# Optimization experiments

Hardware: AMD Instinct MI355X
Metric: run time of the kernel (lower is better)

The kernel has to match this reference:

```python
import jax, jax.numpy as jnp
import numpy as np
import math

N = 30000        # nodes
E = 390000       # edges (first N are self-loops, in node order)
H = 64
NNS = 4          # num_node_states
NES = 4          # num_edge_states
NGRAPH = 64      # graphs in batch
TEMP_ON_EVAL = 1.0


def from_binary(bits):
    # bits: [..., k] of {0,1} -> integer code sum(bits * 2^k)
    pw = (2 ** jnp.arange(bits.shape[-1])).astype(bits.dtype)
    return jnp.sum(bits * pw, axis=-1)


def segment_softmax(logits, seg, num_seg, tau):
    m = jax.ops.segment_max(logits, seg, num_segments=num_seg)
    e = jnp.exp((logits - m[seg]) / tau)
    s = jax.ops.segment_sum(e, seg, num_segments=num_seg)
    return e / s[seg]


def segment_hard_onehot(logits, seg, num_seg):
    # gumbel_softmax with tau=0, no noise: one-hot at per-segment argmax (first on ties)
    n = logits.shape[0]
    m = jax.ops.segment_max(logits, seg, num_segments=num_seg)
    idx = jnp.where(logits >= m[seg], jnp.arange(n, dtype=jnp.int32), jnp.int32(n))
    first = jax.ops.segment_min(idx, seg, num_segments=num_seg)
    return (jnp.arange(n, dtype=jnp.int32) == first[seg]).astype(jnp.int32)


def select_best(emb, bits, scalars, index, num_index):
    # SelectBest with use_select_best=True. states are even ints < 2^(k+1);
    # unique((states, index)) groups == fused key states*num_index+index.
    states = 2 * from_binary(bits)
    key = states * num_index + index
    num_key = (2 ** (bits.shape[-1] + 1)) * num_index
    best = segment_hard_onehot(-scalars[:, 0], key, num_key)
    return emb[states + best]


def temp_by_step(step, upper, lower, num_iter, temp_on_eval):
    if step == -1:
        return temp_on_eval
    frac = min(float(step) / num_iter, 1.0)
    return upper + (lower - upper) * frac


def forward(node_states, edge_states, scalars, edge_index, batch_vec, rev_idx,
            emb_edge, emb_sbv, emb_sbr, emb_static,
            Wq, Wk, Wv, Wek, Wev, Wc, training_step):
    ei0, ei1 = edge_index[0], edge_index[1]
    # self-loop edges are the first N edges in node order ->
    # scalars[edge_index[0]==edge_index[1]] == scalars[:N]
    node_scalars = scalars[:N]                                   # [N,1]

    # select_best_from_virtual
    node_fts = select_best(emb_sbv, node_states, node_scalars, batch_vec, NGRAPH)  # [N,H]
    edge_fts = emb_edge[from_binary(edge_states)]                # [E,H]

    Q = node_fts @ Wq.T
    K = node_fts @ Wk.T
    V = node_fts @ Wv.T

    # combined_edge_KV
    sb = select_best(emb_sbr, node_states[ei0], scalars, ei1, N)  # [E,H]
    edge_K = sb @ Wek.T
    sender_s = node_scalars[ei0]                                  # [E,1]
    reciever_s = node_scalars[ei1]                                # [E,1]
    rlx = (scalars < reciever_s)
    rlx_d = (sender_s + scalars < reciever_s)
    fts = jnp.concatenate([rlx, rlx_d], axis=-1).astype(jnp.int32)  # [E,2] bits
    static_fts = emb_static[from_binary(fts)]                     # [E,H]
    combined = jnp.concatenate([edge_fts, edge_fts[rev_idx], static_fts], axis=1)  # [E,3H]
    edge_V = combined @ Wc.T                                      # [E,H]

    # compute_message
    Qe = Q[ei1]
    Ke = K[ei0] + edge_K
    Ve = V[ei0] + edge_V
    alpha = jnp.sum(Qe * Ke, axis=-1) / math.sqrt(H)              # [E]
    tau = temp_by_step(int(training_step), 3.0, 0.1, 10000, TEMP_ON_EVAL)
    alpha = segment_softmax(alpha, ei1, N, tau)
    message = Ve * alpha[:, None]                                  # [E,H]

    node_out = node_fts + jax.ops.segment_sum(message, ei1, num_segments=N)
    edge_out = edge_fts + message
    return node_out, edge_out


def setup_inputs() -> dict:
    key = jax.random.key(0)
    ks = jax.random.split(key, 16)
    node_states = jax.random.randint(ks[0], (N, NNS), 0, 2, dtype=jnp.int32)
    edge_states = jax.random.randint(ks[1], (E, NES), 0, 2, dtype=jnp.int32)
    scalars = jax.random.normal(ks[2], (E, 1), dtype=jnp.float32)
    loops = jnp.arange(N, dtype=jnp.int32)
    senders = jax.random.randint(ks[3], (E - N,), 0, N, dtype=jnp.int32)
    receivers = jax.random.randint(ks[4], (E - N,), 0, N, dtype=jnp.int32)
    edge_index = jnp.stack([jnp.concatenate([loops, senders]),
                            jnp.concatenate([loops, receivers])])  # [2,E]
    batch_vec = jnp.sort(jax.random.randint(ks[5], (N,), 0, NGRAPH, dtype=jnp.int32))
    rev_idx = jax.random.permutation(ks[6], E).astype(jnp.int32)
    s = 0.05
    return {
        'node_states': node_states, 'edge_states': edge_states, 'scalars': scalars,
        'edge_index': edge_index, 'batch_vec': batch_vec, 'rev_idx': rev_idx,
        'emb_edge': s * jax.random.normal(ks[7], (2 ** NES, H), dtype=jnp.float32),
        'emb_sbv': s * jax.random.normal(ks[8], (2 ** (NNS + 1), H), dtype=jnp.float32),
        'emb_sbr': s * jax.random.normal(ks[9], (2 ** (NNS + 1), H), dtype=jnp.float32),
        'emb_static': s * jax.random.normal(ks[10], (4, H), dtype=jnp.float32),
        'Wq': s * jax.random.normal(ks[11], (H, H), dtype=jnp.float32),
        'Wk': s * jax.random.normal(ks[12], (H, H), dtype=jnp.float32),
        'Wv': s * jax.random.normal(ks[13], (H, H), dtype=jnp.float32),
        'Wek': s * jax.random.normal(ks[14], (H, H), dtype=jnp.float32),
        'Wev': s * jax.random.normal(ks[15], (H, H), dtype=jnp.float32),
        'Wc': s * jax.random.normal(jax.random.fold_in(key, 99), (H, 3 * H), dtype=jnp.float32),
        'training_step': -1,
    }


def reference(node_states, edge_states, scalars, edge_index, batch_vec, rev_idx,
              emb_edge, emb_sbv, emb_sbr, emb_static,
              Wq, Wk, Wv, Wek, Wev, Wc, training_step):
    return forward(node_states, edge_states, scalars, edge_index, batch_vec, rev_idx,
                   emb_edge, emb_sbv, emb_sbr, emb_static,
                   Wq, Wk, Wv, Wek, Wev, Wc, training_step)
```

## Files before the change

### kernel.cpp

```cpp
#include <hip/hip_runtime.h>

#define NN 30000
#define NE 390000
#define HH 64
#define NGRAPH 64
#define AGG_BLOCKS 1024
#define NB 118

__device__ __forceinline__ unsigned sortable_f32(float f) {
    unsigned u = __float_as_uint(f);
    return (u & 0x80000000u) ? ~u : (u | 0x80000000u);
}

#define T_V   0
#define T_C1  2048
#define T_C2  3072
#define T_C3  4096
#define T_A   4352
#define T_B   5376
#define T_Q   6400
#define T_K   8448
#define T_EK  10496

__global__ void k_tab1(const float* __restrict__ emb_sbv, const float* __restrict__ emb_sbr,
                       const float* __restrict__ emb_edge, const float* __restrict__ emb_static,
                       const float* __restrict__ Wq, const float* __restrict__ Wk,
                       const float* __restrict__ Wv, const float* __restrict__ Wek,
                       const float* __restrict__ Wc, float* __restrict__ tabs) {
    int idx = blockIdx.x * 256 + threadIdx.x;
    if (idx >= 10496) return;
    float acc = 0.f;
    if (idx < 2048) {
        int r = idx >> 6, h = idx & 63;
        for (int j = 0; j < 64; ++j) acc += emb_sbv[r*64+j] * Wv[h*64+j];
        tabs[T_V + idx] = acc;
    } else if (idx < 3072) {
        int t = idx - 2048; int r = t >> 6, h = t & 63;
        for (int j = 0; j < 64; ++j) acc += emb_edge[r*64+j] * Wc[h*192+j];
        tabs[T_C1 + t] = acc;
    } else if (idx < 4096) {
        int t = idx - 3072; int r = t >> 6, h = t & 63;
        for (int j = 0; j < 64; ++j) acc += emb_edge[r*64+j] * Wc[h*192+64+j];
        tabs[T_C2 + t] = acc;
    } else if (idx < 4352) {
        int t = idx - 4096; int r = t >> 6, h = t & 63;
        for (int j = 0; j < 64; ++j) acc += emb_static[r*64+j] * Wc[h*192+128+j];
        tabs[T_C3 + t] = acc;
    } else if (idx < 6400) {
        int t = idx - 4352; int r = t >> 6, h = t & 63;
        for (int j = 0; j < 64; ++j) acc += emb_sbv[r*64+j] * Wq[h*64+j];
        tabs[T_Q + t] = acc;
    } else if (idx < 8448) {
        int t = idx - 6400; int r = t >> 6, h = t & 63;
        for (int j = 0; j < 64; ++j) acc += emb_sbv[r*64+j] * Wk[h*64+j];
        tabs[T_K + t] = acc;
    } else {
        int t = idx - 8448; int r = t >> 6, h = t & 63;
        for (int j = 0; j < 64; ++j) acc += emb_sbr[r*64+j] * Wek[h*64+j];
        tabs[T_EK + t] = acc;
    }
}

__global__ void k_tab2(float* __restrict__ tabs) {
    int idx = blockIdx.x * 256 + threadIdx.x;
    if (idx >= 2048) return;
    const float* TQ = tabs + T_Q;
    float acc = 0.f;
    if (idx < 1024) {
        int r1 = idx >> 5, r0 = idx & 31;
        const float* TK = tabs + T_K;
        for (int j = 0; j < 64; ++j) acc += TQ[r1*64+j] * TK[r0*64+j];
        tabs[T_A + idx] = acc * 0.125f;
    } else {
        int t = idx - 1024; int r1 = t >> 5, rk = t & 31;
        const float* TEK = tabs + T_EK;
        for (int j = 0; j < 64; ++j) acc += TQ[r1*64+j] * TEK[rk*64+j];
        tabs[T_B + t] = acc * 0.125f;
    }
}

__global__ void k_node1(const int4* __restrict__ node_states, const float* __restrict__ scalars,
                        const int* __restrict__ batch_vec, int* __restrict__ ns,
                        unsigned long long* __restrict__ nodeSel) {
    int i = blockIdx.x * 256 + threadIdx.x;
    if (i >= NN) return;
    int4 b = node_states[i];
    int st = 2 * (b.x + 2*b.y + 4*b.z + 8*b.w);
    ns[i] = st;
    int key = (st >> 1) * NGRAPH + batch_vec[i];
    unsigned long long pk = ((unsigned long long)sortable_f32(scalars[i]) << 32) | (unsigned)i;
    atomicMin(&nodeSel[key], pk);
}

__global__ void k_edge1(const int4* __restrict__ edge_states, const float* __restrict__ scalars,
                        const int* __restrict__ ei0, const int* __restrict__ ei1,
                        unsigned char* __restrict__ esi,
                        unsigned* __restrict__ cnt, unsigned* __restrict__ rank) {
    int e = blockIdx.x * 256 + threadIdx.x;
    if (e >= NE) return;
    int4 b = edge_states[e];
    int es = b.x + 2*b.y + 4*b.z + 8*b.w;
    float sc = scalars[e];
    int s0 = ei0[e], s1 = ei1[e];
    float send = scalars[s0], recv = scalars[s1];
    int si = (sc < recv ? 1 : 0) + (send + sc < recv ? 2 : 0);
    esi[e] = (unsigned char)(es | (si << 4));
    rank[e] = atomicAdd(&cnt[s1], 1u);
}

__global__ __launch_bounds__(256) void k_bsum(const unsigned* __restrict__ cnt,
                                              unsigned* __restrict__ bsum) {
    __shared__ unsigned red[256];
    int t = threadIdx.x;
    int i = blockIdx.x * 256 + t;
    red[t] = (i < NN) ? cnt[i] : 0u;
    __syncthreads();
    for (int o = 128; o > 0; o >>= 1) {
        if (t < o) red[t] += red[t + o];
        __syncthreads();
    }
    if (t == 0) bsum[blockIdx.x] = red[0];
}

__global__ __launch_bounds__(128) void k_sscan(const unsigned* __restrict__ bsum,
                                               unsigned* __restrict__ bbase,
                                               unsigned* __restrict__ base) {
    __shared__ unsigned s[128];
    int t = threadIdx.x;
    unsigned v = (t < NB) ? bsum[t] : 0u;
    s[t] = v;
    __syncthreads();
    for (int o = 1; o < 128; o <<= 1) {
        unsigned u = (t >= o) ? s[t - o] : 0u;
        __syncthreads();
        s[t] += u;
        __syncthreads();
    }
    if (t < NB) bbase[t] = s[t] - v;
    if (t == 127) { bbase[NB] = s[127]; base[NN] = s[127]; }
}

__global__ __launch_bounds__(256) void k_base(const unsigned* __restrict__ cnt,
        const unsigned* __restrict__ bbase, unsigned* __restrict__ base,
        const int* __restrict__ ns, const int* __restrict__ batch_vec,
        const unsigned long long* __restrict__ nodeSel, int* __restrict__ rowArr) {
    __shared__ unsigned s[256];
    int t = threadIdx.x;
    int i = blockIdx.x * 256 + t;
    unsigned v = (i < NN) ? cnt[i] : 0u;
    s[t] = v;
    __syncthreads();
    for (int o = 1; o < 256; o <<= 1) {
        unsigned u = (t >= o) ? s[t - o] : 0u;
        __syncthreads();
        s[t] += u;
        __syncthreads();
    }
    if (i < NN) {
        base[i] = bbase[blockIdx.x] + s[t] - v;
        int st = ns[i];
        int key = (st >> 1) * NGRAPH + batch_vec[i];
        unsigned win = (unsigned)(nodeSel[key] & 0xffffffffull);
        rowArr[i] = st + (win == (unsigned)i ? 1 : 0);
    }
}

__global__ __launch_bounds__(256) void k_edge2(const int* __restrict__ ei0,
        const int* __restrict__ ei1, const int* __restrict__ rowArr,
        const unsigned char* __restrict__ esi, const int* __restrict__ rev_idx,
        const float* __restrict__ scalars, const unsigned* __restrict__ base,
        const unsigned* __restrict__ rank, uint2* __restrict__ sKey,
        float* __restrict__ sScal) {
    int e = blockIdx.x * 256 + threadIdx.x;
    if (e >= NE) return;
    int s0 = ei0[e], s1 = ei1[e];
    unsigned r0w = (unsigned)rowArr[s0];
    unsigned stq = (r0w & ~1u) >> 1;
    unsigned inf = esi[e];
    unsigned infr = esi[rev_idx[e]];
    unsigned pos = base[s1] + rank[e];
    sKey[pos] = make_uint2((unsigned)e | (r0w << 19) | ((inf & 15u) << 24) | ((infr & 15u) << 28),
                           stq | ((inf >> 4) << 4));
    sScal[pos] = scalars[e];
}

__global__ __launch_bounds__(256) void k_agg(
        const unsigned* __restrict__ base, const uint2* __restrict__ sKey,
        const float* __restrict__ sScal, const int* __restrict__ rowArr,
        const float* __restrict__ tabs, const float* __restrict__ emb_edge,
        const float* __restrict__ emb_sbv, const int* __restrict__ step_ptr,
        float* __restrict__ out_node, float* __restrict__ out_edge) {
    __shared__ float lds[9472];
    __shared__ unsigned scr[4][32];
    int tid = threadIdx.x;
    for (int j = tid; j < 6400; j += 256) lds[j] = tabs[j];
    for (int j = tid; j < 1024; j += 256) lds[6400 + j] = emb_edge[j];
    for (int j = tid; j < 2048; j += 256) lds[7424 + j] = emb_sbv[j];
    __syncthreads();
    int step = step_ptr[0];
    float invTau;
    if (step == -1) invTau = 1.0f;
    else { float frac = fminf((float)step / 10000.f, 1.f); invTau = 1.0f / (3.0f + (0.1f - 3.0f) * frac); }
    int wid = tid >> 6, lane = tid & 63;
    unsigned* mySc = scr[wid];
    unsigned* myE  = scr[wid] + 16;
    int q = lane >> 4, cidx = (lane & 15) << 2;
    for (int i = blockIdx.x * 4 + wid; i < NN; i += AGG_BLOCKS * 4) {
        unsigned j0 = base[i], j1 = base[i + 1];
        int d = (int)(j1 - j0);
        int r1 = rowArr[i];
        const float* Arow = lds + T_A + r1 * 32;
        const float* Brow = lds + T_B + r1 * 32;
        float4 acc = {0.f, 0.f, 0.f, 0.f};
        if (lane < 16) { mySc[lane] = 0xffffffffu; myE[lane] = 0xffffffffu; }
        __builtin_amdgcn_sched_barrier(0);
        if (d > 0 && d <= 64) {
            bool act = lane < d;
            uint2 key = act ? sKey[j0 + lane] : make_uint2(0u, 0u);
            float sc  = act ? sScal[j0 + lane] : 0.f;
            unsigned scs = sortable_f32(sc);
            unsigned g = key.y & 15u;
            unsigned e19 = key.x & 0x7ffffu;
            if (act) atomicMin(&mySc[g], scs);
            __builtin_amdgcn_sched_barrier(0);
            unsigned ms = mySc[g];
            if (act && scs == ms) atomicMin(&myE[g], e19);
            __builtin_amdgcn_sched_barrier(0);
            bool win = act && (myE[g] == e19);
            int r0 = (key.x >> 19) & 31;
            int ekrow = ((int)(key.y & 15u) << 1) + (win ? 1 : 0);
            float ex = act ? __expf((Arow[r0] + Brow[ekrow]) * invTau) : 0.f;
            float s = ex;
            #pragma unroll
            for (int o = 1; o < 64; o <<= 1) s += __shfl_xor(s, o);
            float p = ex / s;
            int nIt = (d + 3) >> 2;
            for (int it = 0; it < nIt; ++it) {
                int jj = it * 4 + q;
                unsigned kx = __shfl(key.x, jj);
                unsigned ky = (unsigned)__shfl((int)key.y, jj);
                float pp = __shfl(p, jj);
                if (jj < d) {
                    unsigned e = kx & 0x7ffffu;
                    int rr0 = (kx >> 19) & 31, es = (kx >> 24) & 15, esr = (kx >> 28) & 15;
                    int si = (ky >> 4) & 3;
                    float4 tv = *(const float4*)&lds[(rr0 << 6) + cidx];
                    float4 c1 = *(const float4*)&lds[T_C1 + (es << 6) + cidx];
                    float4 c2 = *(const float4*)&lds[T_C2 + (esr << 6) + cidx];
                    float4 c3 = *(const float4*)&lds[T_C3 + (si << 6) + cidx];
                    float4 ee = *(const float4*)&lds[6400 + (es << 6) + cidx];
                    float4 o;
                    o.x = pp * (tv.x + c1.x + c2.x + c3.x);
                    o.y = pp * (tv.y + c1.y + c2.y + c3.y);
                    o.z = pp * (tv.z + c1.z + c2.z + c3.z);
                    o.w = pp * (tv.w + c1.w + c2.w + c3.w);
                    acc.x += o.x; acc.y += o.y; acc.z += o.z; acc.w += o.w;
                    o.x += ee.x; o.y += ee.y; o.z += ee.z; o.w += ee.w;
                    *(float4*)&out_edge[(size_t)e * 64 + cidx] = o;
                }
            }
        } else if (d > 64) {
            for (unsigned c = j0; c < j1; c += 64) {
                unsigned j = c + lane;
                if (j < j1) {
                    uint2 key = sKey[j];
                    atomicMin(&mySc[key.y & 15u], sortable_f32(sScal[j]));
                }
            }
            __builtin_amdgcn_sched_barrier(0);
            for (unsigned c = j0; c < j1; c += 64) {
                unsigned j = c + lane;
                if (j < j1) {
                    uint2 key = sKey[j];
                    unsigned g = key.y & 15u;
                    if (sortable_f32(sScal[j]) == mySc[g]) atomicMin(&myE[g], key.x & 0x7ffffu);
                }
            }
            __builtin_amdgcn_sched_barrier(0);
            float s = 0.f;
            for (unsigned c = j0; c < j1; c += 64) {
                unsigned j = c + lane;
                if (j < j1) {
                    uint2 key = sKey[j];
                    bool win = (myE[key.y & 15u] == (key.x & 0x7ffffu));
                    int r0 = (key.x >> 19) & 31;
                    int ekrow = ((int)(key.y & 15u) << 1) + (win ? 1 : 0);
                    s += __expf((Arow[r0] + Brow[ekrow]) * invTau);
                }
            }
            #pragma unroll
            for (int o = 1; o < 64; o <<= 1) s += __shfl_xor(s, o);
            float invS = 1.f / s;
            for (unsigned c = j0; c < j1; c += 4) {
                unsigned j = c + q;
                if (j < j1) {
                    uint2 key = sKey[j];
                    bool win = (myE[key.y & 15u] == (key.x & 0x7ffffu));
                    int r0 = (key.x >> 19) & 31;
                    int ekrow = ((int)(key.y & 15u) << 1) + (win ? 1 : 0);
                    float pp = __expf((Arow[r0] + Brow[ekrow]) * invTau) * invS;
                    unsigned e = key.x & 0x7ffffu;
                    int es = (key.x >> 24) & 15, esr = (key.x >> 28) & 15, si = (key.y >> 4) & 3;
                    float4 tv = *(const float4*)&lds[(r0 << 6) + cidx];
                    float4 c1 = *(const float4*)&lds[T_C1 + (es << 6) + cidx];
                    float4 c2 = *(const float4*)&lds[T_C2 + (esr << 6) + cidx];
                    float4 c3 = *(const float4*)&lds[T_C3 + (si << 6) + cidx];
                    float4 ee = *(const float4*)&lds[6400 + (es << 6) + cidx];
                    float4 o;
                    o.x = pp * (tv.x + c1.x + c2.x + c3.x);
                    o.y = pp * (tv.y + c1.y + c2.y + c3.y);
                    o.z = pp * (tv.z + c1.z + c2.z + c3.z);
                    o.w = pp * (tv.w + c1.w + c2.w + c3.w);
                    acc.x += o.x; acc.y += o.y; acc.z += o.z; acc.w += o.w;
                    o.x += ee.x; o.y += ee.y; o.z += ee.z; o.w += ee.w;
                    *(float4*)&out_edge[(size_t)e * 64 + cidx] = o;
                }
            }
        }
        acc.x += __shfl_xor(acc.x, 16); acc.y += __shfl_xor(acc.y, 16);
        acc.z += __shfl_xor(acc.z, 16); acc.w += __shfl_xor(acc.w, 16);
        acc.x += __shfl_xor(acc.x, 32); acc.y += __shfl_xor(acc.y, 32);
        acc.z += __shfl_xor(acc.z, 32); acc.w += __shfl_xor(acc.w, 32);
        if (lane < 16) {
            float4 nb = *(const float4*)&lds[7424 + (r1 << 6) + cidx];
            float4 o;
            o.x = nb.x + acc.x; o.y = nb.y + acc.y; o.z = nb.z + acc.z; o.w = nb.w + acc.w;
            *(float4*)&out_node[(size_t)i * 64 + cidx] = o;
        }
    }
}

extern "C" void kernel_launch(void* const* d_in, const int* in_sizes, int n_in,
                              void* d_out, int out_size, void* d_ws, size_t ws_size,
                              hipStream_t stream) {
    const int4*  node_states = (const int4*)d_in[0];
    const int4*  edge_states = (const int4*)d_in[1];
    const float* scalars     = (const float*)d_in[2];
    const int*   edge_index  = (const int*)d_in[3];
    const int*   batch_vec   = (const int*)d_in[4];
    const int*   rev_idx     = (const int*)d_in[5];
    const float* emb_edge    = (const float*)d_in[6];
    const float* emb_sbv     = (const float*)d_in[7];
    const float* emb_sbr     = (const float*)d_in[8];
    const float* emb_static  = (const float*)d_in[9];
    const float* Wq  = (const float*)d_in[10];
    const float* Wk  = (const float*)d_in[11];
    const float* Wv  = (const float*)d_in[12];
    const float* Wek = (const float*)d_in[13];
    const float* Wc  = (const float*)d_in[15];
    const int*   step = (const int*)d_in[16];

    const int* ei0 = edge_index;
    const int* ei1 = edge_index + NE;

    char* ws = (char*)d_ws;
    int*      ns     = (int*)(ws);
    int*      rowArr = (int*)(ws + 120000);
    unsigned char* esi = (unsigned char*)(ws + 240000);
    unsigned* rank   = (unsigned*)(ws + 630000);
    unsigned* cnt    = (unsigned*)(ws + 2190000);
    unsigned* baseA  = (unsigned*)(ws + 2310080);
    uint2*    sKey   = (uint2*)(ws + 2430144);
    float*    sScal  = (float*)(ws + 5550144);
    unsigned long long* nodeSel = (unsigned long long*)(ws + 7110144);
    float*    tabs   = (float*)(ws + 7118336);
    unsigned* bsum   = (unsigned*)(ws + 7168512);
    unsigned* bbase  = (unsigned*)(ws + 7169024);

    float* out_node = (float*)d_out;
    float* out_edge = out_node + (size_t)NN * HH;

    hipMemsetAsync(cnt, 0, NN * 4, stream);
    hipMemsetAsync(nodeSel, 0xFF, 1024 * 8, stream);

    hipLaunchKernelGGL(k_tab1, dim3(41), dim3(256), 0, stream,
                       emb_sbv, emb_sbr, emb_edge, emb_static, Wq, Wk, Wv, Wek, Wc, tabs);
    hipLaunchKernelGGL(k_tab2, dim3(8), dim3(256), 0, stream, tabs);

    int nb_node = NB;
    int nb_edge = (NE + 255) / 256;

    hipLaunchKernelGGL(k_node1, dim3(nb_node), dim3(256), 0, stream,
                       node_states, scalars, batch_vec, ns, nodeSel);
    hipLaunchKernelGGL(k_edge1, dim3(nb_edge), dim3(256), 0, stream,
                       edge_states, scalars, ei0, ei1, esi, cnt, rank);
    hipLaunchKernelGGL(k_bsum, dim3(NB), dim3(256), 0, stream, cnt, bsum);
    hipLaunchKernelGGL(k_sscan, dim3(1), dim3(128), 0, stream, bsum, bbase, baseA);
    hipLaunchKernelGGL(k_base, dim3(NB), dim3(256), 0, stream,
                       cnt, bbase, baseA, ns, batch_vec, nodeSel, rowArr);
    hipLaunchKernelGGL(k_edge2, dim3(nb_edge), dim3(256), 0, stream,
                       ei0, ei1, rowArr, esi, rev_idx, scalars, baseA, rank, sKey, sScal);
    hipLaunchKernelGGL(k_agg, dim3(AGG_BLOCKS), dim3(256), 0, stream,
                       baseA, sKey, sScal, rowArr, tabs, emb_edge, emb_sbv, step,
                       out_node, out_edge);
}
```

Measured before the change: 92.83 us.

## Merge preprocessing kernels into phased launches and move edge-side compute into aggregation

Collapses the table, node and edge preprocessing kernels plus the two memsets into three multi-role launches (init, phase2, phase3), cutting launch count and serial dependencies. Node row and scalar are packed into one uint2 per node. The sender scalar now rides in the sort key, so the aggregation kernel computes the static-index bits instead of the edge pass gathering sender and receiver scalars. The group id is derived from the row bits. The cost is extra ALU work inside the aggregation kernel and tighter coupling of key bit layouts.

```diff
diff --git a/kernel.cpp b/kernel.cpp
--- a/kernel.cpp
+++ b/kernel.cpp
@@ -5,7 +5,8 @@
 #define HH 64
 #define NGRAPH 64
 #define AGG_BLOCKS 1024
-#define NB 118
+#define NE_BLK 1524
+#define NN_BLK 118
 
 __device__ __forceinline__ unsigned sortable_f32(float f) {
     unsigned u = __float_as_uint(f);
@@ -22,104 +23,131 @@
 #define T_K   8448
 #define T_EK  10496
 
-__global__ void k_tab1(const float* __restrict__ emb_sbv, const float* __restrict__ emb_sbr,
-                       const float* __restrict__ emb_edge, const float* __restrict__ emb_static,
-                       const float* __restrict__ Wq, const float* __restrict__ Wk,
-                       const float* __restrict__ Wv, const float* __restrict__ Wek,
-                       const float* __restrict__ Wc, float* __restrict__ tabs) {
-    int idx = blockIdx.x * 256 + threadIdx.x;
-    if (idx >= 10496) return;
-    float acc = 0.f;
-    if (idx < 2048) {
-        int r = idx >> 6, h = idx & 63;
-        for (int j = 0; j < 64; ++j) acc += emb_sbv[r*64+j] * Wv[h*64+j];
-        tabs[T_V + idx] = acc;
-    } else if (idx < 3072) {
-        int t = idx - 2048; int r = t >> 6, h = t & 63;
-        for (int j = 0; j < 64; ++j) acc += emb_edge[r*64+j] * Wc[h*192+j];
-        tabs[T_C1 + t] = acc;
-    } else if (idx < 4096) {
-        int t = idx - 3072; int r = t >> 6, h = t & 63;
-        for (int j = 0; j < 64; ++j) acc += emb_edge[r*64+j] * Wc[h*192+64+j];
-        tabs[T_C2 + t] = acc;
-    } else if (idx < 4352) {
-        int t = idx - 4096; int r = t >> 6, h = t & 63;
-        for (int j = 0; j < 64; ++j) acc += emb_static[r*64+j] * Wc[h*192+128+j];
-        tabs[T_C3 + t] = acc;
-    } else if (idx < 6400) {
-        int t = idx - 4352; int r = t >> 6, h = t & 63;
-        for (int j = 0; j < 64; ++j) acc += emb_sbv[r*64+j] * Wq[h*64+j];
-        tabs[T_Q + t] = acc;
-    } else if (idx < 8448) {
-        int t = idx - 6400; int r = t >> 6, h = t & 63;
-        for (int j = 0; j < 64; ++j) acc += emb_sbv[r*64+j] * Wk[h*64+j];
-        tabs[T_K + t] = acc;
+__global__ __launch_bounds__(256) void k_init(
+        const int4* __restrict__ edge_states, const int4* __restrict__ node_states,
+        const float* __restrict__ emb_sbv, const float* __restrict__ emb_sbr,
+        const float* __restrict__ emb_edge, const float* __restrict__ emb_static,
+        const float* __restrict__ Wq, const float* __restrict__ Wk,
+        const float* __restrict__ Wv, const float* __restrict__ Wek,
+        const float* __restrict__ Wc,
+        unsigned char* __restrict__ esi, int* __restrict__ ns,
+        unsigned* __restrict__ cnt, unsigned long long* __restrict__ nodeSel,
+        float* __restrict__ tabs) {
+    int b = blockIdx.x, t = threadIdx.x;
+    if (b < NE_BLK) {
+        int e = b * 256 + t;
+        if (e < NE) {
+            int4 v = edge_states[e];
+            esi[e] = (unsigned char)(v.x + 2*v.y + 4*v.z + 8*v.w);
+        }
+    } else if (b < NE_BLK + NN_BLK) {
+        int i = (b - NE_BLK) * 256 + t;
+        if (i < NN) {
+            int4 v = node_states[i];
+            ns[i] = 2 * (v.x + 2*v.y + 4*v.z + 8*v.w);
+            cnt[i] = 0u;
+        }
+    } else if (b < NE_BLK + NN_BLK + 41) {
+        int idx = (b - NE_BLK - NN_BLK) * 256 + t;
+        if (idx >= 10496) return;
+        float acc = 0.f;
+        if (idx < 2048) {
+            int r = idx >> 6, h = idx & 63;
+            for (int j = 0; j < 64; ++j) acc += emb_sbv[r*64+j] * Wv[h*64+j];
+            tabs[T_V + idx] = acc;
+        } else if (idx < 3072) {
+            int x = idx - 2048; int r = x >> 6, h = x & 63;
+            for (int j = 0; j < 64; ++j) acc += emb_edge[r*64+j] * Wc[h*192+j];
+            tabs[T_C1 + x] = acc;
+        } else if (idx < 4096) {
+            int x = idx - 3072; int r = x >> 6, h = x & 63;
+            for (int j = 0; j < 64; ++j) acc += emb_edge[r*64+j] * Wc[h*192+64+j];
+            tabs[T_C2 + x] = acc;
+        } else if (idx < 4352) {
+            int x = idx - 4096; int r = x >> 6, h = x & 63;
+            for (int j = 0; j < 64; ++j) acc += emb_static[r*64+j] * Wc[h*192+128+j];
+            tabs[T_C3 + x] = acc;
+        } else if (idx < 6400) {
+            int x = idx - 4352; int r = x >> 6, h = x & 63;
+            for (int j = 0; j < 64; ++j) acc += emb_sbv[r*64+j] * Wq[h*64+j];
+            tabs[T_Q + x] = acc;
+        } else if (idx < 8448) {
+            int x = idx - 6400; int r = x >> 6, h = x & 63;
+            for (int j = 0; j < 64; ++j) acc += emb_sbv[r*64+j] * Wk[h*64+j];
+            tabs[T_K + x] = acc;
+        } else {
+            int x = idx - 8448; int r = x >> 6, h = x & 63;
+            for (int j = 0; j < 64; ++j) acc += emb_sbr[r*64+j] * Wek[h*64+j];
+            tabs[T_EK + x] = acc;
+        }
     } else {
-        int t = idx - 8448; int r = t >> 6, h = t & 63;
-        for (int j = 0; j < 64; ++j) acc += emb_sbr[r*64+j] * Wek[h*64+j];
-        tabs[T_EK + t] = acc;
-    }
-}
-
-__global__ void k_tab2(float* __restrict__ tabs) {
-    int idx = blockIdx.x * 256 + threadIdx.x;
-    if (idx >= 2048) return;
-    const float* TQ = tabs + T_Q;
-    float acc = 0.f;
-    if (idx < 1024) {
-        int r1 = idx >> 5, r0 = idx & 31;
-        const float* TK = tabs + T_K;
-        for (int j = 0; j < 64; ++j) acc += TQ[r1*64+j] * TK[r0*64+j];
-        tabs[T_A + idx] = acc * 0.125f;
+        #pragma unroll
+        for (int k = 0; k < 4; ++k) nodeSel[t * 4 + k] = ~0ull;
+    }
+}
+
+__global__ __launch_bounds__(256) void k_phase2(
+        const int* __restrict__ ei1, unsigned* __restrict__ cnt,
+        unsigned* __restrict__ rank, const int* __restrict__ ns,
+        const int* __restrict__ batch_vec, const float* __restrict__ scalars,
+        unsigned long long* __restrict__ nodeSel, float* __restrict__ tabs) {
+    int b = blockIdx.x, t = threadIdx.x;
+    if (b < NE_BLK) {
+        int e = b * 256 + t;
+        if (e < NE) rank[e] = atomicAdd(&cnt[ei1[e]], 1u);
+    } else if (b < NE_BLK + NN_BLK) {
+        int i = (b - NE_BLK) * 256 + t;
+        if (i < NN) {
+            int st = ns[i];
+            int key = (st >> 1) * NGRAPH + batch_vec[i];
+            unsigned long long pk = ((unsigned long long)sortable_f32(scalars[i]) << 32) | (unsigned)i;
+            atomicMin(&nodeSel[key], pk);
+        }
     } else {
-        int t = idx - 1024; int r1 = t >> 5, rk = t & 31;
-        const float* TEK = tabs + T_EK;
-        for (int j = 0; j < 64; ++j) acc += TQ[r1*64+j] * TEK[rk*64+j];
-        tabs[T_B + t] = acc * 0.125f;
-    }
-}
-
-__global__ void k_node1(const int4* __restrict__ node_states, const float* __restrict__ scalars,
-                        const int* __restrict__ batch_vec, int* __restrict__ ns,
-                        unsigned long long* __restrict__ nodeSel) {
-    int i = blockIdx.x * 256 + threadIdx.x;
-    if (i >= NN) return;
-    int4 b = node_states[i];
-    int st = 2 * (b.x + 2*b.y + 4*b.z + 8*b.w);
-    ns[i] = st;
-    int key = (st >> 1) * NGRAPH + batch_vec[i];
-    unsigned long long pk = ((unsigned long long)sortable_f32(scalars[i]) << 32) | (unsigned)i;
-    atomicMin(&nodeSel[key], pk);
-}
-
-__global__ void k_edge1(const int4* __restrict__ edge_states, const float* __restrict__ scalars,
-                        const int* __restrict__ ei0, const int* __restrict__ ei1,
-                        unsigned char* __restrict__ esi,
-                        unsigned* __restrict__ cnt, unsigned* __restrict__ rank) {
-    int e = blockIdx.x * 256 + threadIdx.x;
-    if (e >= NE) return;
-    int4 b = edge_states[e];
-    int es = b.x + 2*b.y + 4*b.z + 8*b.w;
-    float sc = scalars[e];
-    int s0 = ei0[e], s1 = ei1[e];
-    float send = scalars[s0], recv = scalars[s1];
-    int si = (sc < recv ? 1 : 0) + (send + sc < recv ? 2 : 0);
-    esi[e] = (unsigned char)(es | (si << 4));
-    rank[e] = atomicAdd(&cnt[s1], 1u);
-}
-
-__global__ __launch_bounds__(256) void k_bsum(const unsigned* __restrict__ cnt,
-                                              unsigned* __restrict__ bsum) {
-    __shared__ unsigned red[256];
-    int t = threadIdx.x;
-    int i = blockIdx.x * 256 + t;
-    red[t] = (i < NN) ? cnt[i] : 0u;
-    __syncthreads();
-    for (int o = 128; o > 0; o >>= 1) {
-        if (t < o) red[t] += red[t + o];
+        int idx = (b - NE_BLK - NN_BLK) * 256 + t;
+        if (idx >= 2048) return;
+        const float* TQ = tabs + T_Q;
+        float acc = 0.f;
+        if (idx < 1024) {
+            int r1 = idx >> 5, r0 = idx & 31;
+            const float* TK = tabs + T_K;
+            for (int j = 0; j < 64; ++j) acc += TQ[r1*64+j] * TK[r0*64+j];
+            tabs[T_A + idx] = acc * 0.125f;
+        } else {
+            int x = idx - 1024; int r1 = x >> 5, rk = x & 31;
+            const float* TEK = tabs + T_EK;
+            for (int j = 0; j < 64; ++j) acc += TQ[r1*64+j] * TEK[rk*64+j];
+            tabs[T_B + x] = acc * 0.125f;
+        }
+    }
+}
+
+__global__ __launch_bounds__(256) void k_phase3(
+        const unsigned* __restrict__ cnt, unsigned* __restrict__ bsum,
+        const int* __restrict__ ns, const int* __restrict__ batch_vec,
+        const unsigned long long* __restrict__ nodeSel,
+        const float* __restrict__ scalars, uint2* __restrict__ nodePk) {
+    int b = blockIdx.x, t = threadIdx.x;
+    if (b < NN_BLK) {
+        __shared__ unsigned red[256];
+        int i = b * 256 + t;
+        red[t] = (i < NN) ? cnt[i] : 0u;
         __syncthreads();
-    }
-    if (t == 0) bsum[blockIdx.x] = red[0];
+        for (int o = 128; o > 0; o >>= 1) {
+            if (t < o) red[t] += red[t + o];
+            __syncthreads();
+        }
+        if (t == 0) bsum[b] = red[0];
+    } else {
+        int i = (b - NN_BLK) * 256 + t;
+        if (i < NN) {
+            int st = ns[i];
+            int key = (st >> 1) * NGRAPH + batch_vec[i];
+            unsigned win = (unsigned)(nodeSel[key] & 0xffffffffull);
+            unsigned row = (unsigned)st + (win == (unsigned)i ? 1u : 0u);
+            nodePk[i] = make_uint2(row, __float_as_uint(scalars[i]));
+        }
+    }
 }
 
 __global__ __launch_bounds__(128) void k_sscan(const unsigned* __restrict__ bsum,
@@ -127,7 +155,7 @@
                                                unsigned* __restrict__ base) {
     __shared__ unsigned s[128];
     int t = threadIdx.x;
-    unsigned v = (t < NB) ? bsum[t] : 0u;
+    unsigned v = (t < NN_BLK) ? bsum[t] : 0u;
     s[t] = v;
     __syncthreads();
     for (int o = 1; o < 128; o <<= 1) {
@@ -136,14 +164,12 @@
         s[t] += u;
         __syncthreads();
     }
-    if (t < NB) bbase[t] = s[t] - v;
-    if (t == 127) { bbase[NB] = s[127]; base[NN] = s[127]; }
+    if (t < NN_BLK) bbase[t] = s[t] - v;
+    if (t == 127) { bbase[NN_BLK] = s[127]; base[NN] = s[127]; }
 }
 
 __global__ __launch_bounds__(256) void k_base(const unsigned* __restrict__ cnt,
-        const unsigned* __restrict__ bbase, unsigned* __restrict__ base,
-        const int* __restrict__ ns, const int* __restrict__ batch_vec,
-        const unsigned long long* __restrict__ nodeSel, int* __restrict__ rowArr) {
+        const unsigned* __restrict__ bbase, unsigned* __restrict__ base) {
     __shared__ unsigned s[256];
     int t = threadIdx.x;
     int i = blockIdx.x * 256 + t;
@@ -156,17 +182,11 @@
         s[t] += u;
         __syncthreads();
     }
-    if (i < NN) {
-        base[i] = bbase[blockIdx.x] + s[t] - v;
-        int st = ns[i];
-        int key = (st >> 1) * NGRAPH + batch_vec[i];
-        unsigned win = (unsigned)(nodeSel[key] & 0xffffffffull);
-        rowArr[i] = st + (win == (unsigned)i ? 1 : 0);
-    }
+    if (i < NN) base[i] = bbase[blockIdx.x] + s[t] - v;
 }
 
 __global__ __launch_bounds__(256) void k_edge2(const int* __restrict__ ei0,
-        const int* __restrict__ ei1, const int* __restrict__ rowArr,
+        const int* __restrict__ ei1, const uint2* __restrict__ nodePk,
         const unsigned char* __restrict__ esi, const int* __restrict__ rev_idx,
         const float* __restrict__ scalars, const unsigned* __restrict__ base,
         const unsigned* __restrict__ rank, uint2* __restrict__ sKey,
@@ -174,19 +194,17 @@
     int e = blockIdx.x * 256 + threadIdx.x;
     if (e >= NE) return;
     int s0 = ei0[e], s1 = ei1[e];
-    unsigned r0w = (unsigned)rowArr[s0];
-    unsigned stq = (r0w & ~1u) >> 1;
-    unsigned inf = esi[e];
-    unsigned infr = esi[rev_idx[e]];
+    uint2 np = nodePk[s0];
+    unsigned es = esi[e];
+    unsigned esr = esi[rev_idx[e]];
     unsigned pos = base[s1] + rank[e];
-    sKey[pos] = make_uint2((unsigned)e | (r0w << 19) | ((inf & 15u) << 24) | ((infr & 15u) << 28),
-                           stq | ((inf >> 4) << 4));
+    sKey[pos] = make_uint2((unsigned)e | (np.x << 19) | (es << 24) | (esr << 28), np.y);
     sScal[pos] = scalars[e];
 }
 
 __global__ __launch_bounds__(256) void k_agg(
         const unsigned* __restrict__ base, const uint2* __restrict__ sKey,
-        const float* __restrict__ sScal, const int* __restrict__ rowArr,
+        const float* __restrict__ sScal, const uint2* __restrict__ nodePk,
         const float* __restrict__ tabs, const float* __restrict__ emb_edge,
         const float* __restrict__ emb_sbv, const int* __restrict__ step_ptr,
         float* __restrict__ out_node, float* __restrict__ out_edge) {
@@ -208,7 +226,9 @@
     for (int i = blockIdx.x * 4 + wid; i < NN; i += AGG_BLOCKS * 4) {
         unsigned j0 = base[i], j1 = base[i + 1];
         int d = (int)(j1 - j0);
-        int r1 = rowArr[i];
+        uint2 np = nodePk[i];
+        int r1 = (int)np.x;
+        float recv = __uint_as_float(np.y);
         const float* Arow = lds + T_A + r1 * 32;
         const float* Brow = lds + T_B + r1 * 32;
         float4 acc = {0.f, 0.f, 0.f, 0.f};
@@ -219,7 +239,7 @@
             uint2 key = act ? sKey[j0 + lane] : make_uint2(0u, 0u);
             float sc  = act ? sScal[j0 + lane] : 0.f;
             unsigned scs = sortable_f32(sc);
-            unsigned g = key.y & 15u;
+            unsigned g = (key.x >> 20) & 15u;
             unsigned e19 = key.x & 0x7ffffu;
             if (act) atomicMin(&mySc[g], scs);
             __builtin_amdgcn_sched_barrier(0);
@@ -228,8 +248,10 @@
             __builtin_amdgcn_sched_barrier(0);
             bool win = act && (myE[g] == e19);
             int r0 = (key.x >> 19) & 31;
-            int ekrow = ((int)(key.y & 15u) << 1) + (win ? 1 : 0);
+            int ekrow = (r0 & 30) + (win ? 1 : 0);
             float ex = act ? __expf((Arow[r0] + Brow[ekrow]) * invTau) : 0.f;
+            float send = __uint_as_float(key.y);
+            int si = (sc < recv ? 1 : 0) + (send + sc < recv ? 2 : 0);
             float s = ex;
             #pragma unroll
             for (int o = 1; o < 64; o <<= 1) s += __shfl_xor(s, o);
@@ -238,16 +260,15 @@
             for (int it = 0; it < nIt; ++it) {
                 int jj = it * 4 + q;
                 unsigned kx = __shfl(key.x, jj);
-                unsigned ky = (unsigned)__shfl((int)key.y, jj);
+                int sii = __shfl(si, jj);
                 float pp = __shfl(p, jj);
                 if (jj < d) {
                     unsigned e = kx & 0x7ffffu;
                     int rr0 = (kx >> 19) & 31, es = (kx >> 24) & 15, esr = (kx >> 28) & 15;
-                    int si = (ky >> 4) & 3;
                     float4 tv = *(const float4*)&lds[(rr0 << 6) + cidx];
                     float4 c1 = *(const float4*)&lds[T_C1 + (es << 6) + cidx];
                     float4 c2 = *(const float4*)&lds[T_C2 + (esr << 6) + cidx];
-                    float4 c3 = *(const float4*)&lds[T_C3 + (si << 6) + cidx];
+                    float4 c3 = *(const float4*)&lds[T_C3 + (sii << 6) + cidx];
                     float4 ee = *(const float4*)&lds[6400 + (es << 6) + cidx];
                     float4 o;
                     o.x = pp * (tv.x + c1.x + c2.x + c3.x);
@@ -264,7 +285,7 @@
                 unsigned j = c + lane;
                 if (j < j1) {
                     uint2 key = sKey[j];
-                    atomicMin(&mySc[key.y & 15u], sortable_f32(sScal[j]));
+                    atomicMin(&mySc[(key.x >> 20) & 15u], sortable_f32(sScal[j]));
                 }
             }
             __builtin_amdgcn_sched_barrier(0);
@@ -272,7 +293,7 @@
                 unsigned j = c + lane;
                 if (j < j1) {
                     uint2 key = sKey[j];
-                    unsigned g = key.y & 15u;
+                    unsigned g = (key.x >> 20) & 15u;
                     if (sortable_f32(sScal[j]) == mySc[g]) atomicMin(&myE[g], key.x & 0x7ffffu);
                 }
             }
@@ -282,9 +303,9 @@
                 unsigned j = c + lane;
                 if (j < j1) {
                     uint2 key = sKey[j];
-                    bool win = (myE[key.y & 15u] == (key.x & 0x7ffffu));
+                    bool win = (myE[(key.x >> 20) & 15u] == (key.x & 0x7ffffu));
                     int r0 = (key.x >> 19) & 31;
-                    int ekrow = ((int)(key.y & 15u) << 1) + (win ? 1 : 0);
+                    int ekrow = (r0 & 30) + (win ? 1 : 0);
                     s += __expf((Arow[r0] + Brow[ekrow]) * invTau);
                 }
             }
@@ -295,12 +316,15 @@
                 unsigned j = c + q;
                 if (j < j1) {
                     uint2 key = sKey[j];
-                    bool win = (myE[key.y & 15u] == (key.x & 0x7ffffu));
+                    float sc = sScal[j];
+                    bool win = (myE[(key.x >> 20) & 15u] == (key.x & 0x7ffffu));
                     int r0 = (key.x >> 19) & 31;
-                    int ekrow = ((int)(key.y & 15u) << 1) + (win ? 1 : 0);
+                    int ekrow = (r0 & 30) + (win ? 1 : 0);
                     float pp = __expf((Arow[r0] + Brow[ekrow]) * invTau) * invS;
+                    float send = __uint_as_float(key.y);
+                    int si = (sc < recv ? 1 : 0) + (send + sc < recv ? 2 : 0);
                     unsigned e = key.x & 0x7ffffu;
-                    int es = (key.x >> 24) & 15, esr = (key.x >> 28) & 15, si = (key.y >> 4) & 3;
+                    int es = (key.x >> 24) & 15, esr = (key.x >> 28) & 15;
                     float4 tv = *(const float4*)&lds[(r0 << 6) + cidx];
                     float4 c1 = *(const float4*)&lds[T_C1 + (es << 6) + cidx];
                     float4 c2 = *(const float4*)&lds[T_C2 + (esr << 6) + cidx];
@@ -355,42 +379,33 @@
 
     char* ws = (char*)d_ws;
     int*      ns     = (int*)(ws);
-    int*      rowArr = (int*)(ws + 120000);
-    unsigned char* esi = (unsigned char*)(ws + 240000);
-    unsigned* rank   = (unsigned*)(ws + 630000);
-    unsigned* cnt    = (unsigned*)(ws + 2190000);
-    unsigned* baseA  = (unsigned*)(ws + 2310080);
-    uint2*    sKey   = (uint2*)(ws + 2430144);
-    float*    sScal  = (float*)(ws + 5550144);
-    unsigned long long* nodeSel = (unsigned long long*)(ws + 7110144);
-    float*    tabs   = (float*)(ws + 7118336);
-    unsigned* bsum   = (unsigned*)(ws + 7168512);
-    unsigned* bbase  = (unsigned*)(ws + 7169024);
+    uint2*    nodePk = (uint2*)(ws + 120000);
+    unsigned char* esi = (unsigned char*)(ws + 360000);
+    unsigned* rank   = (unsigned*)(ws + 750016);
+    unsigned* cnt    = (unsigned*)(ws + 2310016);
+    unsigned* baseA  = (unsigned*)(ws + 2430080);
+    uint2*    sKey   = (uint2*)(ws + 2550144);
+    float*    sScal  = (float*)(ws + 5670144);
+    unsigned long long* nodeSel = (unsigned long long*)(ws + 7230144);
+    float*    tabs   = (float*)(ws + 7238336);
+    unsigned* bsum   = (unsigned*)(ws + 7288512);
+    unsigned* bbase  = (unsigned*)(ws + 7289024);
 
     float* out_node = (float*)d_out;
     float* out_edge = out_node + (size_t)NN * HH;
 
-    hipMemsetAsync(cnt, 0, NN * 4, stream);
-    hipMemsetAsync(nodeSel, 0xFF, 1024 * 8, stream);
-
-    hipLaunchKernelGGL(k_tab1, dim3(41), dim3(256), 0, stream,
-                       emb_sbv, emb_sbr, emb_edge, emb_static, Wq, Wk, Wv, Wek, Wc, tabs);
-    hipLaunchKernelGGL(k_tab2, dim3(8), dim3(256), 0, stream, tabs);
-
-    int nb_node = NB;
-    int nb_edge = (NE + 255) / 256;
-
-    hipLaunchKernelGGL(k_node1, dim3(nb_node), dim3(256), 0, stream,
-                       node_states, scalars, batch_vec, ns, nodeSel);
-    hipLaunchKernelGGL(k_edge1, dim3(nb_edge), dim3(256), 0, stream,
-                       edge_states, scalars, ei0, ei1, esi, cnt, rank);
-    hipLaunchKernelGGL(k_bsum, dim3(NB), dim3(256), 0, stream, cnt, bsum);
+    hipLaunchKernelGGL(k_init, dim3(NE_BLK + NN_BLK + 41 + 1), dim3(256), 0, stream,
+                       edge_states, node_states, emb_sbv, emb_sbr, emb_edge, emb_static,
+                       Wq, Wk, Wv, Wek, Wc, esi, ns, cnt, nodeSel, tabs);
+    hipLaunchKernelGGL(k_phase2, dim3(NE_BLK + NN_BLK + 8), dim3(256), 0, stream,
+                       ei1, cnt, rank, ns, batch_vec, scalars, nodeSel, tabs);
+    hipLaunchKernelGGL(k_phase3, dim3(NN_BLK * 2), dim3(256), 0, stream,
+                       cnt, bsum, ns, batch_vec, nodeSel, scalars, nodePk);
     hipLaunchKernelGGL(k_sscan, dim3(1), dim3(128), 0, stream, bsum, bbase, baseA);
-    hipLaunchKernelGGL(k_base, dim3(NB), dim3(256), 0, stream,
-                       cnt, bbase, baseA, ns, batch_vec, nodeSel, rowArr);
-    hipLaunchKernelGGL(k_edge2, dim3(nb_edge), dim3(256), 0, stream,
-                       ei0, ei1, rowArr, esi, rev_idx, scalars, baseA, rank, sKey, sScal);
+    hipLaunchKernelGGL(k_base, dim3(NN_BLK), dim3(256), 0, stream, cnt, bbase, baseA);
+    hipLaunchKernelGGL(k_edge2, dim3(NE_BLK), dim3(256), 0, stream,
+                       ei0, ei1, nodePk, esi, rev_idx, scalars, baseA, rank, sKey, sScal);
     hipLaunchKernelGGL(k_agg, dim3(AGG_BLOCKS), dim3(256), 0, stream,
-                       baseA, sKey, sScal, rowArr, tabs, emb_edge, emb_sbv, step,
+                       baseA, sKey, sScal, nodePk, tabs, emb_edge, emb_sbv, step,
                        out_node, out_edge);
 }
```

After: 77.44 us (median of 2 runs). -16.6%, faster.
